# Performance work log

Measured on AMD Instinct MI355X. Metric: run time of the kernel, lower is better.

Reference implementation:

```python
import jax, jax.numpy as jnp
import numpy as np

BN_EPS = 1e-5


def setup_inputs() -> dict:
    key = jax.random.key(0)
    ks = jax.random.split(key, 6)
    b, c_out, c_high = 8, 256, 512
    h1 = w1 = 64
    h2 = w2 = 32
    return {
        "fms_low": jax.random.normal(ks[0], (b, c_out, h1, w1), jnp.float32),
        "fms_high": jax.random.normal(ks[1], (b, c_high, h2, w2), jnp.float32),
        "w_conv": jax.random.normal(ks[2], (c_out, c_high), jnp.float32) * (1.0 / np.sqrt(c_high)),
        "bn_gamma": jnp.ones((c_out,), jnp.float32),
        "bn_beta": jnp.zeros((c_out,), jnp.float32),
        "bn_mean": jnp.zeros((c_out,), jnp.float32),
        "bn_var": jnp.ones((c_out,), jnp.float32),
        "fc1_w": jax.random.normal(ks[3], (c_out // 4, c_out), jnp.float32) * (1.0 / np.sqrt(c_out)),
        "fc1_b": jnp.zeros((c_out // 4,), jnp.float32),
        "fc2_w": jax.random.normal(ks[4], (c_out // 4, c_out), jnp.float32) * (1.0 / np.sqrt(c_out)),
        "fc2_b": jnp.zeros((c_out // 4,), jnp.float32),
        "scale": jax.random.normal(ks[5], (1,), jnp.float32),
    }


def reference(fms_low, fms_high, w_conv, bn_gamma, bn_beta, bn_mean, bn_var,
              fc1_w, fc1_b, fc2_w, fc2_b, scale):
    b, c, h1, w1 = fms_low.shape
    # conv_high: 1x1 conv (no bias) + BN (inference) + ReLU
    x = jnp.einsum('bchw,oc->bohw', fms_high, w_conv)  # [b, 256, h2, w2]
    inv = bn_gamma / jnp.sqrt(bn_var + BN_EPS)
    x = x * inv[None, :, None, None] + (bn_beta - bn_mean * inv)[None, :, None, None]
    x = jax.nn.relu(x)
    # raw row-major reshapes, matching torch .view(b, -1, C)
    feat_low = fms_low.reshape(b, -1, c)    # [b, N_low, 256]
    feat_high = x.reshape(b, -1, c)         # [b, N_high, 256]
    mid_low = feat_low @ fc1_w.T + fc1_b    # [b, N_low, 64]
    mid_high = feat_high @ fc2_w.T + fc2_b  # [b, N_high, 64]
    energy = jnp.einsum('bnd,bmd->bnm', mid_low, mid_high)  # [b, N_low, N_high]
    attn = jax.nn.softmax(energy, axis=-1)
    # bmm(feat_high^T, attn^T) -> [b, 256, N_low]
    mid = jnp.einsum('bmc,bnm->bcn', feat_high, attn).reshape(b, c, h1, w1)
    return scale[0] * mid
```

## Files before the change

kernel.cpp:

```cpp
#include <hip/hip_runtime.h>
#include <hip/hip_bf16.h>

typedef __bf16 v8bf __attribute__((ext_vector_type(8)));
typedef float  v4f  __attribute__((ext_vector_type(4)));

typedef __attribute__((address_space(3))) void       lds_vd;
typedef __attribute__((address_space(1))) const void gbl_vd;

#define MFMA16(a, b, c) __builtin_amdgcn_mfma_f32_16x16x32_bf16(a, b, c, 0, 0, 0)

__device__ __forceinline__ void split_hl(float v, __bf16* h, __bf16* l) {
    __bf16 hh = (__bf16)v;
    *h = hh;
    *l = (__bf16)(v - (float)hh);
}

__device__ __forceinline__ int swz_idx(int row, int col) {
    return row * 64 + ((((col >> 3) ^ (row & 7))) << 3) + (col & 7);
}
__device__ __forceinline__ const __bf16* frag_ptr(const __bf16* base, int row, int g) {
    return base + row * 64 + ((g ^ (row & 7)) << 3);
}


__global__ __launch_bounds__(256) void k_conv(
    const float* __restrict__ FH, const float* __restrict__ W,
    const float* __restrict__ gamma, const float* __restrict__ beta,
    const float* __restrict__ mean, const float* __restrict__ var,
    __bf16* __restrict__ Xhi, __bf16* __restrict__ Xlo, __bf16* __restrict__ VT)
{
    __shared__ __align__(16) __bf16 Ah[2][64 * 64];
    __shared__ __align__(16) __bf16 Al[2][64 * 64];
    __shared__ __align__(16) __bf16 Bh[2][64 * 64];
    __shared__ __align__(16) __bf16 Bl[2][64 * 64];
    __shared__ float invl[64], shl[64];

    const int tid = threadIdx.x, lane = tid & 63, w = tid >> 6;
    const int l15 = lane & 15, quad = lane >> 4;
    const int u0 = blockIdx.x * 16, o0 = blockIdx.y * 64, b = blockIdx.z;
    const float* FHb = FH + (size_t)b * 524288;

    if (tid < 64) {
        const int o = o0 + tid;
        const float iv = gamma[o] * rsqrtf(var[o] + 1e-5f);
        invl[tid] = iv;
        shl[tid] = beta[o] - mean[o] * iv;
    }

    const int ao = tid >> 2, aseg = tid & 3;
    float wreg[16], freg[16];
    {
        const float* wp = W + (size_t)(o0 + ao) * 512 + aseg * 16;
        #pragma unroll
        for (int q = 0; q < 4; ++q) {
            float4 f = ((const float4*)wp)[q];
            wreg[4*q] = f.x; wreg[4*q+1] = f.y; wreg[4*q+2] = f.z; wreg[4*q+3] = f.w;
        }
        const float* fp = FHb + (size_t)lane * 1024 + w * 256 + u0;
        #pragma unroll
        for (int q = 0; q < 4; ++q) {
            float4 f = ((const float4*)fp)[q];
            freg[4*q] = f.x; freg[4*q+1] = f.y; freg[4*q+2] = f.z; freg[4*q+3] = f.w;
        }
    }

    v4f acc[2][2];
    #pragma unroll
    for (int i = 0; i < 2; ++i)
        #pragma unroll
        for (int j = 0; j < 2; ++j) { v4f z = {0.f,0.f,0.f,0.f}; acc[i][j] = z; }
    const int oh = w >> 1, nh = w & 1;

    for (int ch = 0; ch < 8; ++ch) {
        const int bf = ch & 1;
        #pragma unroll
        for (int z = 0; z < 2; ++z) {
            v8bf hv, lv;
            #pragma unroll
            for (int e = 0; e < 8; ++e) {
                __bf16 h, l; split_hl(wreg[8*z + e], &h, &l);
                hv[e] = h; lv[e] = l;
            }
            const int gi = (2*aseg + z) ^ (ao & 7);
            *(v8bf*)(Ah[bf] + ao*64 + (gi << 3)) = hv;
            *(v8bf*)(Al[bf] + ao*64 + (gi << 3)) = lv;
        }
        #pragma unroll
        for (int ul = 0; ul < 16; ++ul) {
            __bf16 h, l; split_hl(freg[ul], &h, &l);
            const int idx = (w*16 + ul)*64 + (((lane >> 3) ^ (ul & 7)) << 3) + (lane & 7);
            Bh[bf][idx] = h; Bl[bf][idx] = l;
        }
        __syncthreads();
        if (ch < 7) {
            const int c1 = (ch + 1) * 64;
            const float* wp = W + (size_t)(o0 + ao) * 512 + c1 + aseg * 16;
            #pragma unroll
            for (int q = 0; q < 4; ++q) {
                float4 f = ((const float4*)wp)[q];
                wreg[4*q] = f.x; wreg[4*q+1] = f.y; wreg[4*q+2] = f.z; wreg[4*q+3] = f.w;
            }
            const float* fp = FHb + (size_t)(c1 + lane) * 1024 + w * 256 + u0;
            #pragma unroll
            for (int q = 0; q < 4; ++q) {
                float4 f = ((const float4*)fp)[q];
                freg[4*q] = f.x; freg[4*q+1] = f.y; freg[4*q+2] = f.z; freg[4*q+3] = f.w;
            }
        }
        #pragma unroll
        for (int ks = 0; ks < 2; ++ks) {
            const int g = 4*ks + quad;
            v8bf a_h[2], a_l[2], b_h[2], b_l[2];
            #pragma unroll
            for (int i = 0; i < 2; ++i) {
                const int row = oh*32 + i*16 + l15;
                a_h[i] = *(const v8bf*)frag_ptr(Ah[bf], row, g);
                a_l[i] = *(const v8bf*)frag_ptr(Al[bf], row, g);
            }
            #pragma unroll
            for (int j = 0; j < 2; ++j) {
                const int row = nh*32 + j*16 + l15;
                b_h[j] = *(const v8bf*)frag_ptr(Bh[bf], row, g);
                b_l[j] = *(const v8bf*)frag_ptr(Bl[bf], row, g);
            }
            #pragma unroll
            for (int i = 0; i < 2; ++i)
                #pragma unroll
                for (int j = 0; j < 2; ++j) {
                    acc[i][j] = MFMA16(a_h[i], b_h[j], acc[i][j]);
                    acc[i][j] = MFMA16(a_h[i], b_l[j], acc[i][j]);
                    acc[i][j] = MFMA16(a_l[i], b_h[j], acc[i][j]);
                }
        }
    }
    __syncthreads();

    #pragma unroll
    for (int i = 0; i < 2; ++i)
        #pragma unroll
        for (int j = 0; j < 2; ++j)
            #pragma unroll
            for (int r = 0; r < 4; ++r) {
                const int row = oh*32 + i*16 + quad*4 + r;
                const int col = nh*32 + j*16 + l15;
                float v = acc[i][j][r] * invl[row] + shl[row];
                v = fmaxf(v, 0.f);
                __bf16 h, l; split_hl(v, &h, &l);
                const int idx = swz_idx(row, col);
                Ah[0][idx] = h; Al[0][idx] = l;
            }
    __syncthreads();
    {
        const int o = tid >> 2, pv = tid & 3;
        const size_t gbase = ((size_t)b*256 + o0 + o) * 1024 + pv*256 + u0;
        #pragma unroll
        for (int z = 0; z < 2; ++z) {
            const int gi = (2*pv + z) ^ (o & 7);
            v8bf h = *(v8bf*)(Ah[0] + o*64 + (gi << 3));
            v8bf l = *(v8bf*)(Al[0] + o*64 + (gi << 3));
            *(v8bf*)(Xhi + gbase + z*8) = h;
            *(v8bf*)(Xlo + gbase + z*8) = l;
        }
    }
    {
        const int ul = tid >> 4, s = tid & 15;
        __bf16 tmp[16];
        #pragma unroll
        for (int k = 0; k < 16; ++k) {
            const int m = s*16 + k;
            const int row = m >> 2;
            const int col = (m & 3)*16 + ul;
            tmp[k] = Ah[0][swz_idx(row, col)];
        }
        __bf16* vp = VT + ((size_t)b*256 + u0 + ul) * 1024 + 4*o0 + s*16;
        *(v8bf*)(vp)     = *(v8bf*)(tmp);
        *(v8bf*)(vp + 8) = *(v8bf*)(tmp + 8);
    }
}

__global__ __launch_bounds__(256) void k_proj32(
    const float* __restrict__ Feat, const float* __restrict__ Wfc,
    const float* __restrict__ bfc,
    __bf16* __restrict__ Ohi, __bf16* __restrict__ Olo)
{
    __shared__ __align__(16) __bf16 Wh[64 * 256], Wl[64 * 256];
    const int tid = threadIdx.x, lane = tid & 63, w = tid >> 6;
    const int l15 = lane & 15, quad = lane >> 4;
    const int r0 = blockIdx.x * 64;

    {
        const int row = tid >> 2, seg = tid & 3;
        const float* wp = Wfc + (size_t)row * 256 + seg * 64;
        #pragma unroll
        for (int z = 0; z < 8; ++z) {
            float4 f0 = ((const float4*)wp)[2*z];
            float4 f1 = ((const float4*)wp)[2*z + 1];
            float e[8] = {f0.x, f0.y, f0.z, f0.w, f1.x, f1.y, f1.z, f1.w};
            v8bf hv, lv;
            #pragma unroll
            for (int k = 0; k < 8; ++k) { __bf16 h, l; split_hl(e[k], &h, &l); hv[k] = h; lv[k] = l; }
            const int slot = (seg*8 + z) ^ (row & 7);
            *(v8bf*)(Wh + row*256 + (slot << 3)) = hv;
            *(v8bf*)(Wl + row*256 + (slot << 3)) = lv;
        }
    }
    __syncthreads();

    const float* ap = Feat + (size_t)(r0 + w*16 + l15) * 256;
    v4f acc[4];
    #pragma unroll
    for (int j = 0; j < 4; ++j) { v4f z = {0.f,0.f,0.f,0.f}; acc[j] = z; }

    #pragma unroll
    for (int ks = 0; ks < 8; ++ks) {
        float4 f0 = *(const float4*)(ap + ks*32 + quad*8);
        float4 f1 = *(const float4*)(ap + ks*32 + quad*8 + 4);
        float e[8] = {f0.x, f0.y, f0.z, f0.w, f1.x, f1.y, f1.z, f1.w};
        v8bf ah, al;
        #pragma unroll
        for (int k = 0; k < 8; ++k) { __bf16 h, l; split_hl(e[k], &h, &l); ah[k] = h; al[k] = l; }
        const int gk = ks*4 + quad;
        #pragma unroll
        for (int j = 0; j < 4; ++j) {
            const int row = j*16 + l15;
            const int slot = gk ^ (row & 7);
            v8bf bh = *(const v8bf*)(Wh + row*256 + (slot << 3));
            v8bf bl = *(const v8bf*)(Wl + row*256 + (slot << 3));
            acc[j] = MFMA16(ah, bh, acc[j]);
            acc[j] = MFMA16(ah, bl, acc[j]);
            acc[j] = MFMA16(al, bh, acc[j]);
        }
    }
    #pragma unroll
    for (int j = 0; j < 4; ++j) {
        const float bias = bfc[j*16 + l15];
        #pragma unroll
        for (int r = 0; r < 4; ++r) {
            const int orow = r0 + w*16 + quad*4 + r;
            __bf16 h, l; split_hl(acc[j][r] + bias, &h, &l);
            Ohi[(size_t)orow*64 + j*16 + l15] = h;
            Olo[(size_t)orow*64 + j*16 + l15] = l;
        }
    }
}

__global__ __launch_bounds__(256) void k_projbf(
    const __bf16* __restrict__ Fhi, const __bf16* __restrict__ Flo,
    const float* __restrict__ Wfc, const float* __restrict__ bfc,
    __bf16* __restrict__ Ohi, __bf16* __restrict__ Olo)
{
    __shared__ __align__(16) __bf16 Wh[64 * 256], Wl[64 * 256];
    const int tid = threadIdx.x, lane = tid & 63, w = tid >> 6;
    const int l15 = lane & 15, quad = lane >> 4;
    const int r0 = blockIdx.x * 64;

    {
        const int row = tid >> 2, seg = tid & 3;
        const float* wp = Wfc + (size_t)row * 256 + seg * 64;
        #pragma unroll
        for (int z = 0; z < 8; ++z) {
            float4 f0 = ((const float4*)wp)[2*z];
            float4 f1 = ((const float4*)wp)[2*z + 1];
            float e[8] = {f0.x, f0.y, f0.z, f0.w, f1.x, f1.y, f1.z, f1.w};
            v8bf hv, lv;
            #pragma unroll
            for (int k = 0; k < 8; ++k) { __bf16 h, l; split_hl(e[k], &h, &l); hv[k] = h; lv[k] = l; }
            const int slot = (seg*8 + z) ^ (row & 7);
            *(v8bf*)(Wh + row*256 + (slot << 3)) = hv;
            *(v8bf*)(Wl + row*256 + (slot << 3)) = lv;
        }
    }
    __syncthreads();

    const __bf16* aph = Fhi + (size_t)(r0 + w*16 + l15) * 256;
    const __bf16* apl = Flo + (size_t)(r0 + w*16 + l15) * 256;
    v4f acc[4];
    #pragma unroll
    for (int j = 0; j < 4; ++j) { v4f z = {0.f,0.f,0.f,0.f}; acc[j] = z; }

    #pragma unroll
    for (int ks = 0; ks < 8; ++ks) {
        v8bf ah = *(const v8bf*)(aph + ks*32 + quad*8);
        v8bf al = *(const v8bf*)(apl + ks*32 + quad*8);
        const int gk = ks*4 + quad;
        #pragma unroll
        for (int j = 0; j < 4; ++j) {
            const int row = j*16 + l15;
            const int slot = gk ^ (row & 7);
            v8bf bh = *(const v8bf*)(Wh + row*256 + (slot << 3));
            v8bf bl = *(const v8bf*)(Wl + row*256 + (slot << 3));
            acc[j] = MFMA16(ah, bh, acc[j]);
            acc[j] = MFMA16(ah, bl, acc[j]);
            acc[j] = MFMA16(al, bh, acc[j]);
        }
    }
    #pragma unroll
    for (int j = 0; j < 4; ++j) {
        const float bias = bfc[j*16 + l15];
        #pragma unroll
        for (int r = 0; r < 4; ++r) {
            const int orow = r0 + w*16 + quad*4 + r;
            __bf16 h, l; split_hl(acc[j][r] + bias, &h, &l);
            Ohi[(size_t)orow*64 + j*16 + l15] = h;
            Olo[(size_t)orow*64 + j*16 + l15] = l;
        }
    }
}

__global__ __launch_bounds__(256) void k_attn(
    const __bf16* __restrict__ MLhi, const __bf16* __restrict__ MLlo,
    const __bf16* __restrict__ MHhi, const __bf16* __restrict__ MHlo,
    const __bf16* __restrict__ VT,
    const float* __restrict__ scale_p,
    float* __restrict__ out)
{
    __shared__ __align__(16) __bf16 Khi[2][32 * 64];
    __shared__ __align__(16) __bf16 Klo[2][32 * 64];
    __shared__ __align__(16) __bf16 Vs[2][256 * 32];

    const int tid = threadIdx.x, lane = tid & 63, w = tid >> 6;
    const int l15 = lane & 15, quad = lane >> 4;
    const int b = blockIdx.x & 7, qtb = blockIdx.x >> 3;
    const int q0 = qtb * 64;

    v8bf qhi[2], qlo[2];
    {
        const __bf16* qp  = MLhi + ((size_t)(b*4096 + q0 + w*16 + l15)) * 64;
        const __bf16* qlp = MLlo + ((size_t)(b*4096 + q0 + w*16 + l15)) * 64;
        #pragma unroll
        for (int h = 0; h < 2; ++h) {
            qhi[h] = *(const v8bf*)(qp + h*32 + quad*8);
            qlo[h] = *(const v8bf*)(qlp + h*32 + quad*8);
        }
    }

    const char* Khg = (const char*)(MHhi + (size_t)b * 65536);
    const char* Klg = (const char*)(MHlo + (size_t)b * 65536);
    const char* Vg  = (const char*)(VT + (size_t)b * 262144);
    const int offK = (lane >> 3) * 128 + (((lane & 7) ^ ((lane >> 3) & 7)) << 4);
    const int offV = (lane >> 2) * 2048 + ((((lane & 3) ^ ((lane >> 3) & 3))) << 4);

    v4f oacc[16];
    #pragma unroll
    for (int ct = 0; ct < 16; ++ct) { v4f z = {0.f,0.f,0.f,0.f}; oacc[ct] = z; }
    float lrow = 0.f;

    const int srcA = l15 + (((2*quad) & 3) << 4);
    const int srcB = l15 + (((2*quad + 1) & 3) << 4);
    const bool hi_mb = ((quad >> 1) & 1) != 0;

    {
        __builtin_amdgcn_global_load_lds((gbl_vd*)(Khg + w*1024 + offK),
                                         (lds_vd*)((char*)Khi[0] + w*1024), 16, 0, 0);
        __builtin_amdgcn_global_load_lds((gbl_vd*)(Klg + w*1024 + offK),
                                         (lds_vd*)((char*)Klo[0] + w*1024), 16, 0, 0);
        for (int i = w; i < 16; i += 4)
            __builtin_amdgcn_global_load_lds((gbl_vd*)(Vg + i*32768 + offV),
                                             (lds_vd*)((char*)Vs[0] + i*1024), 16, 0, 0);
    }

    for (int ch = 0; ch < 32; ++ch) {
        const int bf = ch & 1;
        __syncthreads();
        if (ch < 31) {
            const int m0 = (ch + 1) * 32, nb = bf ^ 1;
            __builtin_amdgcn_global_load_lds((gbl_vd*)(Khg + m0*128 + w*1024 + offK),
                                             (lds_vd*)((char*)Khi[nb] + w*1024), 16, 0, 0);
            __builtin_amdgcn_global_load_lds((gbl_vd*)(Klg + m0*128 + w*1024 + offK),
                                             (lds_vd*)((char*)Klo[nb] + w*1024), 16, 0, 0);
            for (int i = w; i < 16; i += 4)
                __builtin_amdgcn_global_load_lds((gbl_vd*)(Vg + m0*2 + i*32768 + offV),
                                                 (lds_vd*)((char*)Vs[nb] + i*1024), 16, 0, 0);
        }

        v4f s0 = {0.f,0.f,0.f,0.f}, s1 = {0.f,0.f,0.f,0.f};
        #pragma unroll
        for (int h = 0; h < 2; ++h) {
            const int g = h*4 + quad;
            v8bf kh0 = *(const v8bf*)frag_ptr(Khi[bf], l15,      g);
            v8bf kl0 = *(const v8bf*)frag_ptr(Klo[bf], l15,      g);
            v8bf kh1 = *(const v8bf*)frag_ptr(Khi[bf], 16 + l15, g);
            v8bf kl1 = *(const v8bf*)frag_ptr(Klo[bf], 16 + l15, g);
            s0 = MFMA16(kh0, qhi[h], s0);
            s0 = MFMA16(kl0, qhi[h], s0);
            s0 = MFMA16(kh0, qlo[h], s0);
            s1 = MFMA16(kh1, qhi[h], s1);
            s1 = MFMA16(kl1, qhi[h], s1);
            s1 = MFMA16(kh1, qlo[h], s1);
        }

        float P0[4], P1[4];
        #pragma unroll
        for (int r = 0; r < 4; ++r) {
            P0[r] = __expf(s0[r]);
            P1[r] = __expf(s1[r]);
            lrow += P0[r] + P1[r];
        }

        v8bf pf;
        #pragma unroll
        for (int r = 0; r < 4; ++r) {
            const float a0 = __shfl(P0[r], srcA, 64);
            const float a1 = __shfl(P1[r], srcA, 64);
            pf[r] = (__bf16)(hi_mb ? a1 : a0);
            const float b0 = __shfl(P0[r], srcB, 64);
            const float b1 = __shfl(P1[r], srcB, 64);
            pf[4 + r] = (__bf16)(hi_mb ? b1 : b0);
        }

        #pragma unroll
        for (int ct = 0; ct < 16; ++ct) {
            const int vrow = ct*16 + l15;
            v8bf vv = *(const v8bf*)(Vs[bf] + vrow*32 + ((quad ^ ((vrow >> 1) & 3)) << 3));
            oacc[ct] = MFMA16(vv, pf, oacc[ct]);
        }
    }

    lrow += __shfl_xor(lrow, 16, 64);
    lrow += __shfl_xor(lrow, 32, 64);
    const float invq = scale_p[0] / lrow;

    float* outb = out + (size_t)b * 256 * 4096 + q0 + w*16 + l15;
    #pragma unroll
    for (int ct = 0; ct < 16; ++ct) {
        #pragma unroll
        for (int r = 0; r < 4; ++r) {
            const int c = ct*16 + quad*4 + r;
            outb[(size_t)c * 4096] = oacc[ct][r] * invq;
        }
    }
}

extern "C" void kernel_launch(void* const* d_in, const int* in_sizes, int n_in,
                              void* d_out, int out_size, void* d_ws, size_t ws_size,
                              hipStream_t stream)
{
    const float* fms_low  = (const float*)d_in[0];
    const float* fms_high = (const float*)d_in[1];
    const float* w_conv   = (const float*)d_in[2];
    const float* gamma    = (const float*)d_in[3];
    const float* beta     = (const float*)d_in[4];
    const float* mean     = (const float*)d_in[5];
    const float* var      = (const float*)d_in[6];
    const float* fc1_w    = (const float*)d_in[7];
    const float* fc1_b    = (const float*)d_in[8];
    const float* fc2_w    = (const float*)d_in[9];
    const float* fc2_b    = (const float*)d_in[10];
    const float* scale    = (const float*)d_in[11];
    float* out = (float*)d_out;

    __bf16* Xhi  = (__bf16*)d_ws;
    __bf16* Xlo  = Xhi  + (size_t)8*256*1024;
    __bf16* VT   = Xlo  + (size_t)8*256*1024;
    __bf16* MLhi = VT   + (size_t)8*256*1024;
    __bf16* MLlo = MLhi + (size_t)8*4096*64;
    __bf16* MHhi = MLlo + (size_t)8*4096*64;
    __bf16* MHlo = MHhi + (size_t)8*1024*64;

    k_conv<<<dim3(16, 4, 8), 256, 0, stream>>>(fms_high, w_conv, gamma, beta,
                                               mean, var, Xhi, Xlo, VT);
    k_projbf<<<dim3(128), 256, 0, stream>>>(Xhi, Xlo, fc2_w, fc2_b, MHhi, MHlo);
    k_proj32<<<dim3(512), 256, 0, stream>>>(fms_low, fc1_w, fc1_b, MLhi, MLlo);
    k_attn<<<dim3(512), 256, 0, stream>>>(MLhi, MLlo, MHhi, MHlo, VT, scale, out);
}
```

Baseline: 197.0 us.

## Merge conv and low projection into one launch, split attention over channel halves

The conv+BN+ReLU kernel and the fc1 projection of the low-resolution features are merged into one kernel, with the block index choosing the role. The conv loses its LDS double buffer, and the fc1 weights are staged in two K chunks to shrink LDS. The high projection now uses 32-row blocks, doubling its grid. Attention splits the 256 output channels into two halves per block, doubling the grid and halving accumulators and V staging. This trades more occupancy and parallelism for recomputing QK^T and the softmax in both channel halves, and drops one kernel launch.

```diff
diff --git a/kernel.cpp b/kernel.cpp
--- a/kernel.cpp
+++ b/kernel.cpp
@@ -23,223 +23,227 @@
 }
 
 
-__global__ __launch_bounds__(256) void k_conv(
+__global__ __launch_bounds__(256) void k_prep(
     const float* __restrict__ FH, const float* __restrict__ W,
     const float* __restrict__ gamma, const float* __restrict__ beta,
     const float* __restrict__ mean, const float* __restrict__ var,
-    __bf16* __restrict__ Xhi, __bf16* __restrict__ Xlo, __bf16* __restrict__ VT)
+    const float* __restrict__ Feat,
+    const float* __restrict__ fc1w, const float* __restrict__ fc1b,
+    __bf16* __restrict__ Xhi, __bf16* __restrict__ Xlo, __bf16* __restrict__ VT,
+    __bf16* __restrict__ MLhi, __bf16* __restrict__ MLlo)
 {
-    __shared__ __align__(16) __bf16 Ah[2][64 * 64];
-    __shared__ __align__(16) __bf16 Al[2][64 * 64];
-    __shared__ __align__(16) __bf16 Bh[2][64 * 64];
-    __shared__ __align__(16) __bf16 Bl[2][64 * 64];
-    __shared__ float invl[64], shl[64];
-
+    __shared__ __align__(16) char smem[33280];
     const int tid = threadIdx.x, lane = tid & 63, w = tid >> 6;
     const int l15 = lane & 15, quad = lane >> 4;
-    const int u0 = blockIdx.x * 16, o0 = blockIdx.y * 64, b = blockIdx.z;
-    const float* FHb = FH + (size_t)b * 524288;
-
-    if (tid < 64) {
-        const int o = o0 + tid;
-        const float iv = gamma[o] * rsqrtf(var[o] + 1e-5f);
-        invl[tid] = iv;
-        shl[tid] = beta[o] - mean[o] * iv;
-    }
-
-    const int ao = tid >> 2, aseg = tid & 3;
-    float wreg[16], freg[16];
-    {
-        const float* wp = W + (size_t)(o0 + ao) * 512 + aseg * 16;
-        #pragma unroll
-        for (int q = 0; q < 4; ++q) {
-            float4 f = ((const float4*)wp)[q];
-            wreg[4*q] = f.x; wreg[4*q+1] = f.y; wreg[4*q+2] = f.z; wreg[4*q+3] = f.w;
-        }
-        const float* fp = FHb + (size_t)lane * 1024 + w * 256 + u0;
-        #pragma unroll
-        for (int q = 0; q < 4; ++q) {
-            float4 f = ((const float4*)fp)[q];
-            freg[4*q] = f.x; freg[4*q+1] = f.y; freg[4*q+2] = f.z; freg[4*q+3] = f.w;
-        }
-    }
-
-    v4f acc[2][2];
-    #pragma unroll
-    for (int i = 0; i < 2; ++i)
-        #pragma unroll
-        for (int j = 0; j < 2; ++j) { v4f z = {0.f,0.f,0.f,0.f}; acc[i][j] = z; }
-    const int oh = w >> 1, nh = w & 1;
-
-    for (int ch = 0; ch < 8; ++ch) {
-        const int bf = ch & 1;
-        #pragma unroll
-        for (int z = 0; z < 2; ++z) {
-            v8bf hv, lv;
-            #pragma unroll
-            for (int e = 0; e < 8; ++e) {
-                __bf16 h, l; split_hl(wreg[8*z + e], &h, &l);
-                hv[e] = h; lv[e] = l;
-            }
-            const int gi = (2*aseg + z) ^ (ao & 7);
-            *(v8bf*)(Ah[bf] + ao*64 + (gi << 3)) = hv;
-            *(v8bf*)(Al[bf] + ao*64 + (gi << 3)) = lv;
-        }
-        #pragma unroll
-        for (int ul = 0; ul < 16; ++ul) {
-            __bf16 h, l; split_hl(freg[ul], &h, &l);
-            const int idx = (w*16 + ul)*64 + (((lane >> 3) ^ (ul & 7)) << 3) + (lane & 7);
-            Bh[bf][idx] = h; Bl[bf][idx] = l;
-        }
-        __syncthreads();
-        if (ch < 7) {
-            const int c1 = (ch + 1) * 64;
-            const float* wp = W + (size_t)(o0 + ao) * 512 + c1 + aseg * 16;
+    const int bid = blockIdx.x;
+
+    if (bid < 512) {
+        __bf16* Ah = (__bf16*)smem;
+        __bf16* Al = (__bf16*)(smem + 8192);
+        __bf16* Bh = (__bf16*)(smem + 16384);
+        __bf16* Bl = (__bf16*)(smem + 24576);
+        float* invl = (float*)(smem + 32768);
+        float* shl  = (float*)(smem + 33024);
+
+        const int u0 = (bid & 15) * 16, o0 = ((bid >> 4) & 3) * 64, b = bid >> 6;
+        const float* FHb = FH + (size_t)b * 524288;
+
+        if (tid < 64) {
+            const int o = o0 + tid;
+            const float iv = gamma[o] * rsqrtf(var[o] + 1e-5f);
+            invl[tid] = iv;
+            shl[tid] = beta[o] - mean[o] * iv;
+        }
+
+        const int ao = tid >> 2, aseg = tid & 3;
+        float wreg[16], freg[16];
+        {
+            const float* wp = W + (size_t)(o0 + ao) * 512 + aseg * 16;
             #pragma unroll
             for (int q = 0; q < 4; ++q) {
                 float4 f = ((const float4*)wp)[q];
                 wreg[4*q] = f.x; wreg[4*q+1] = f.y; wreg[4*q+2] = f.z; wreg[4*q+3] = f.w;
             }
-            const float* fp = FHb + (size_t)(c1 + lane) * 1024 + w * 256 + u0;
+            const float* fp = FHb + (size_t)lane * 1024 + w * 256 + u0;
             #pragma unroll
             for (int q = 0; q < 4; ++q) {
                 float4 f = ((const float4*)fp)[q];
                 freg[4*q] = f.x; freg[4*q+1] = f.y; freg[4*q+2] = f.z; freg[4*q+3] = f.w;
             }
         }
-        #pragma unroll
-        for (int ks = 0; ks < 2; ++ks) {
-            const int g = 4*ks + quad;
-            v8bf a_h[2], a_l[2], b_h[2], b_l[2];
-            #pragma unroll
-            for (int i = 0; i < 2; ++i) {
-                const int row = oh*32 + i*16 + l15;
-                a_h[i] = *(const v8bf*)frag_ptr(Ah[bf], row, g);
-                a_l[i] = *(const v8bf*)frag_ptr(Al[bf], row, g);
-            }
-            #pragma unroll
-            for (int j = 0; j < 2; ++j) {
-                const int row = nh*32 + j*16 + l15;
-                b_h[j] = *(const v8bf*)frag_ptr(Bh[bf], row, g);
-                b_l[j] = *(const v8bf*)frag_ptr(Bl[bf], row, g);
-            }
-            #pragma unroll
-            for (int i = 0; i < 2; ++i)
+
+        v4f acc[2][2];
+        #pragma unroll
+        for (int i = 0; i < 2; ++i)
+            #pragma unroll
+            for (int j = 0; j < 2; ++j) { v4f z = {0.f,0.f,0.f,0.f}; acc[i][j] = z; }
+        const int oh = w >> 1, nh = w & 1;
+
+        for (int ch = 0; ch < 8; ++ch) {
+            if (ch) __syncthreads();
+            #pragma unroll
+            for (int z = 0; z < 2; ++z) {
+                v8bf hv, lv;
+                #pragma unroll
+                for (int e = 0; e < 8; ++e) {
+                    __bf16 h, l; split_hl(wreg[8*z + e], &h, &l);
+                    hv[e] = h; lv[e] = l;
+                }
+                const int gi = (2*aseg + z) ^ (ao & 7);
+                *(v8bf*)(Ah + ao*64 + (gi << 3)) = hv;
+                *(v8bf*)(Al + ao*64 + (gi << 3)) = lv;
+            }
+            #pragma unroll
+            for (int ul = 0; ul < 16; ++ul) {
+                __bf16 h, l; split_hl(freg[ul], &h, &l);
+                const int idx = (w*16 + ul)*64 + (((lane >> 3) ^ (ul & 7)) << 3) + (lane & 7);
+                Bh[idx] = h; Bl[idx] = l;
+            }
+            __syncthreads();
+            if (ch < 7) {
+                const int c1 = (ch + 1) * 64;
+                const float* wp = W + (size_t)(o0 + ao) * 512 + c1 + aseg * 16;
+                #pragma unroll
+                for (int q = 0; q < 4; ++q) {
+                    float4 f = ((const float4*)wp)[q];
+                    wreg[4*q] = f.x; wreg[4*q+1] = f.y; wreg[4*q+2] = f.z; wreg[4*q+3] = f.w;
+                }
+                const float* fp = FHb + (size_t)(c1 + lane) * 1024 + w * 256 + u0;
+                #pragma unroll
+                for (int q = 0; q < 4; ++q) {
+                    float4 f = ((const float4*)fp)[q];
+                    freg[4*q] = f.x; freg[4*q+1] = f.y; freg[4*q+2] = f.z; freg[4*q+3] = f.w;
+                }
+            }
+            #pragma unroll
+            for (int ks = 0; ks < 2; ++ks) {
+                const int g = 4*ks + quad;
+                v8bf a_h[2], a_l[2], b_h[2], b_l[2];
+                #pragma unroll
+                for (int i = 0; i < 2; ++i) {
+                    const int row = oh*32 + i*16 + l15;
+                    a_h[i] = *(const v8bf*)frag_ptr(Ah, row, g);
+                    a_l[i] = *(const v8bf*)frag_ptr(Al, row, g);
+                }
                 #pragma unroll
                 for (int j = 0; j < 2; ++j) {
-                    acc[i][j] = MFMA16(a_h[i], b_h[j], acc[i][j]);
-                    acc[i][j] = MFMA16(a_h[i], b_l[j], acc[i][j]);
-                    acc[i][j] = MFMA16(a_l[i], b_h[j], acc[i][j]);
-                }
-        }
-    }
-    __syncthreads();
-
-    #pragma unroll
-    for (int i = 0; i < 2; ++i)
-        #pragma unroll
-        for (int j = 0; j < 2; ++j)
+                    const int row = nh*32 + j*16 + l15;
+                    b_h[j] = *(const v8bf*)frag_ptr(Bh, row, g);
+                    b_l[j] = *(const v8bf*)frag_ptr(Bl, row, g);
+                }
+                #pragma unroll
+                for (int i = 0; i < 2; ++i)
+                    #pragma unroll
+                    for (int j = 0; j < 2; ++j) {
+                        acc[i][j] = MFMA16(a_h[i], b_h[j], acc[i][j]);
+                        acc[i][j] = MFMA16(a_h[i], b_l[j], acc[i][j]);
+                        acc[i][j] = MFMA16(a_l[i], b_h[j], acc[i][j]);
+                    }
+            }
+        }
+        __syncthreads();
+
+        #pragma unroll
+        for (int i = 0; i < 2; ++i)
+            #pragma unroll
+            for (int j = 0; j < 2; ++j)
+                #pragma unroll
+                for (int r = 0; r < 4; ++r) {
+                    const int row = oh*32 + i*16 + quad*4 + r;
+                    const int col = nh*32 + j*16 + l15;
+                    float v = acc[i][j][r] * invl[row] + shl[row];
+                    v = fmaxf(v, 0.f);
+                    __bf16 h, l; split_hl(v, &h, &l);
+                    const int idx = swz_idx(row, col);
+                    Ah[idx] = h; Al[idx] = l;
+                }
+        __syncthreads();
+        {
+            const int o = tid >> 2, pv = tid & 3;
+            const size_t gbase = ((size_t)b*256 + o0 + o) * 1024 + pv*256 + u0;
+            #pragma unroll
+            for (int z = 0; z < 2; ++z) {
+                const int gi = (2*pv + z) ^ (o & 7);
+                v8bf h = *(v8bf*)(Ah + o*64 + (gi << 3));
+                v8bf l = *(v8bf*)(Al + o*64 + (gi << 3));
+                *(v8bf*)(Xhi + gbase + z*8) = h;
+                *(v8bf*)(Xlo + gbase + z*8) = l;
+            }
+        }
+        {
+            const int ul = tid >> 4, s = tid & 15;
+            __bf16 tmp[16];
+            #pragma unroll
+            for (int k = 0; k < 16; ++k) {
+                const int m = s*16 + k;
+                const int row = m >> 2;
+                const int col = (m & 3)*16 + ul;
+                tmp[k] = Ah[swz_idx(row, col)];
+            }
+            __bf16* vp = VT + ((size_t)b*256 + u0 + ul) * 1024 + 4*(bid >> 4 & 3)*64 + s*16;
+            *(v8bf*)(vp)     = *(v8bf*)(tmp);
+            *(v8bf*)(vp + 8) = *(v8bf*)(tmp + 8);
+        }
+    } else {
+        __bf16* Wh = (__bf16*)smem;
+        __bf16* Wl = (__bf16*)(smem + 16384);
+        const int r0 = (bid - 512) * 64;
+        const float* ap = Feat + (size_t)(r0 + w*16 + l15) * 256;
+
+        v4f acc[4];
+        #pragma unroll
+        for (int j = 0; j < 4; ++j) { v4f z = {0.f,0.f,0.f,0.f}; acc[j] = z; }
+
+        for (int kc = 0; kc < 2; ++kc) {
+            if (kc) __syncthreads();
+            {
+                const int row = tid >> 2, seg = tid & 3;
+                const float* wp = fc1w + (size_t)row * 256 + kc*128 + seg * 32;
+                #pragma unroll
+                for (int z = 0; z < 4; ++z) {
+                    float4 f0 = ((const float4*)wp)[2*z];
+                    float4 f1 = ((const float4*)wp)[2*z + 1];
+                    float e[8] = {f0.x, f0.y, f0.z, f0.w, f1.x, f1.y, f1.z, f1.w};
+                    v8bf hv, lv;
+                    #pragma unroll
+                    for (int k = 0; k < 8; ++k) { __bf16 h, l; split_hl(e[k], &h, &l); hv[k] = h; lv[k] = l; }
+                    const int slot = (seg*4 + z) ^ (row & 7);
+                    *(v8bf*)(Wh + row*128 + (slot << 3)) = hv;
+                    *(v8bf*)(Wl + row*128 + (slot << 3)) = lv;
+                }
+            }
+            __syncthreads();
+            #pragma unroll
+            for (int ks = 0; ks < 4; ++ks) {
+                float4 f0 = *(const float4*)(ap + kc*128 + ks*32 + quad*8);
+                float4 f1 = *(const float4*)(ap + kc*128 + ks*32 + quad*8 + 4);
+                float e[8] = {f0.x, f0.y, f0.z, f0.w, f1.x, f1.y, f1.z, f1.w};
+                v8bf ah, al;
+                #pragma unroll
+                for (int k = 0; k < 8; ++k) { __bf16 h, l; split_hl(e[k], &h, &l); ah[k] = h; al[k] = l; }
+                const int gk = ks*4 + quad;
+                #pragma unroll
+                for (int j = 0; j < 4; ++j) {
+                    const int row = j*16 + l15;
+                    const int slot = gk ^ (row & 7);
+                    v8bf bh = *(const v8bf*)(Wh + row*128 + (slot << 3));
+                    v8bf bl = *(const v8bf*)(Wl + row*128 + (slot << 3));
+                    acc[j] = MFMA16(ah, bh, acc[j]);
+                    acc[j] = MFMA16(ah, bl, acc[j]);
+                    acc[j] = MFMA16(al, bh, acc[j]);
+                }
+            }
+        }
+        #pragma unroll
+        for (int j = 0; j < 4; ++j) {
+            const float bias = fc1b[j*16 + l15];
             #pragma unroll
             for (int r = 0; r < 4; ++r) {
-                const int row = oh*32 + i*16 + quad*4 + r;
-                const int col = nh*32 + j*16 + l15;
-                float v = acc[i][j][r] * invl[row] + shl[row];
-                v = fmaxf(v, 0.f);
-                __bf16 h, l; split_hl(v, &h, &l);
-                const int idx = swz_idx(row, col);
-                Ah[0][idx] = h; Al[0][idx] = l;
-            }
-    __syncthreads();
-    {
-        const int o = tid >> 2, pv = tid & 3;
-        const size_t gbase = ((size_t)b*256 + o0 + o) * 1024 + pv*256 + u0;
-        #pragma unroll
-        for (int z = 0; z < 2; ++z) {
-            const int gi = (2*pv + z) ^ (o & 7);
-            v8bf h = *(v8bf*)(Ah[0] + o*64 + (gi << 3));
-            v8bf l = *(v8bf*)(Al[0] + o*64 + (gi << 3));
-            *(v8bf*)(Xhi + gbase + z*8) = h;
-            *(v8bf*)(Xlo + gbase + z*8) = l;
-        }
-    }
-    {
-        const int ul = tid >> 4, s = tid & 15;
-        __bf16 tmp[16];
-        #pragma unroll
-        for (int k = 0; k < 16; ++k) {
-            const int m = s*16 + k;
-            const int row = m >> 2;
-            const int col = (m & 3)*16 + ul;
-            tmp[k] = Ah[0][swz_idx(row, col)];
-        }
-        __bf16* vp = VT + ((size_t)b*256 + u0 + ul) * 1024 + 4*o0 + s*16;
-        *(v8bf*)(vp)     = *(v8bf*)(tmp);
-        *(v8bf*)(vp + 8) = *(v8bf*)(tmp + 8);
-    }
-}
-
-__global__ __launch_bounds__(256) void k_proj32(
-    const float* __restrict__ Feat, const float* __restrict__ Wfc,
-    const float* __restrict__ bfc,
-    __bf16* __restrict__ Ohi, __bf16* __restrict__ Olo)
-{
-    __shared__ __align__(16) __bf16 Wh[64 * 256], Wl[64 * 256];
-    const int tid = threadIdx.x, lane = tid & 63, w = tid >> 6;
-    const int l15 = lane & 15, quad = lane >> 4;
-    const int r0 = blockIdx.x * 64;
-
-    {
-        const int row = tid >> 2, seg = tid & 3;
-        const float* wp = Wfc + (size_t)row * 256 + seg * 64;
-        #pragma unroll
-        for (int z = 0; z < 8; ++z) {
-            float4 f0 = ((const float4*)wp)[2*z];
-            float4 f1 = ((const float4*)wp)[2*z + 1];
-            float e[8] = {f0.x, f0.y, f0.z, f0.w, f1.x, f1.y, f1.z, f1.w};
-            v8bf hv, lv;
-            #pragma unroll
-            for (int k = 0; k < 8; ++k) { __bf16 h, l; split_hl(e[k], &h, &l); hv[k] = h; lv[k] = l; }
-            const int slot = (seg*8 + z) ^ (row & 7);
-            *(v8bf*)(Wh + row*256 + (slot << 3)) = hv;
-            *(v8bf*)(Wl + row*256 + (slot << 3)) = lv;
-        }
-    }
-    __syncthreads();
-
-    const float* ap = Feat + (size_t)(r0 + w*16 + l15) * 256;
-    v4f acc[4];
-    #pragma unroll
-    for (int j = 0; j < 4; ++j) { v4f z = {0.f,0.f,0.f,0.f}; acc[j] = z; }
-
-    #pragma unroll
-    for (int ks = 0; ks < 8; ++ks) {
-        float4 f0 = *(const float4*)(ap + ks*32 + quad*8);
-        float4 f1 = *(const float4*)(ap + ks*32 + quad*8 + 4);
-        float e[8] = {f0.x, f0.y, f0.z, f0.w, f1.x, f1.y, f1.z, f1.w};
-        v8bf ah, al;
-        #pragma unroll
-        for (int k = 0; k < 8; ++k) { __bf16 h, l; split_hl(e[k], &h, &l); ah[k] = h; al[k] = l; }
-        const int gk = ks*4 + quad;
-        #pragma unroll
-        for (int j = 0; j < 4; ++j) {
-            const int row = j*16 + l15;
-            const int slot = gk ^ (row & 7);
-            v8bf bh = *(const v8bf*)(Wh + row*256 + (slot << 3));
-            v8bf bl = *(const v8bf*)(Wl + row*256 + (slot << 3));
-            acc[j] = MFMA16(ah, bh, acc[j]);
-            acc[j] = MFMA16(ah, bl, acc[j]);
-            acc[j] = MFMA16(al, bh, acc[j]);
-        }
-    }
-    #pragma unroll
-    for (int j = 0; j < 4; ++j) {
-        const float bias = bfc[j*16 + l15];
-        #pragma unroll
-        for (int r = 0; r < 4; ++r) {
-            const int orow = r0 + w*16 + quad*4 + r;
-            __bf16 h, l; split_hl(acc[j][r] + bias, &h, &l);
-            Ohi[(size_t)orow*64 + j*16 + l15] = h;
-            Olo[(size_t)orow*64 + j*16 + l15] = l;
+                const int orow = r0 + w*16 + quad*4 + r;
+                __bf16 h, l; split_hl(acc[j][r] + bias, &h, &l);
+                MLhi[(size_t)orow*64 + j*16 + l15] = h;
+                MLlo[(size_t)orow*64 + j*16 + l15] = l;
+            }
         }
     }
 }
@@ -249,60 +253,63 @@
     const float* __restrict__ Wfc, const float* __restrict__ bfc,
     __bf16* __restrict__ Ohi, __bf16* __restrict__ Olo)
 {
-    __shared__ __align__(16) __bf16 Wh[64 * 256], Wl[64 * 256];
+    __shared__ __align__(16) __bf16 Wh[64 * 128], Wl[64 * 128];
     const int tid = threadIdx.x, lane = tid & 63, w = tid >> 6;
     const int l15 = lane & 15, quad = lane >> 4;
-    const int r0 = blockIdx.x * 64;
-
-    {
-        const int row = tid >> 2, seg = tid & 3;
-        const float* wp = Wfc + (size_t)row * 256 + seg * 64;
-        #pragma unroll
-        for (int z = 0; z < 8; ++z) {
-            float4 f0 = ((const float4*)wp)[2*z];
-            float4 f1 = ((const float4*)wp)[2*z + 1];
-            float e[8] = {f0.x, f0.y, f0.z, f0.w, f1.x, f1.y, f1.z, f1.w};
-            v8bf hv, lv;
-            #pragma unroll
-            for (int k = 0; k < 8; ++k) { __bf16 h, l; split_hl(e[k], &h, &l); hv[k] = h; lv[k] = l; }
-            const int slot = (seg*8 + z) ^ (row & 7);
-            *(v8bf*)(Wh + row*256 + (slot << 3)) = hv;
-            *(v8bf*)(Wl + row*256 + (slot << 3)) = lv;
-        }
-    }
-    __syncthreads();
-
-    const __bf16* aph = Fhi + (size_t)(r0 + w*16 + l15) * 256;
-    const __bf16* apl = Flo + (size_t)(r0 + w*16 + l15) * 256;
-    v4f acc[4];
+    const int r0 = blockIdx.x * 32;
+    const int mt = w & 1, dh = w >> 1;
+
+    const __bf16* aph = Fhi + (size_t)(r0 + mt*16 + l15) * 256;
+    const __bf16* apl = Flo + (size_t)(r0 + mt*16 + l15) * 256;
+
+    v4f acc[2];
+    { v4f z = {0.f,0.f,0.f,0.f}; acc[0] = z; acc[1] = z; }
+
+    for (int kc = 0; kc < 2; ++kc) {
+        if (kc) __syncthreads();
+        {
+            const int row = tid >> 2, seg = tid & 3;
+            const float* wp = Wfc + (size_t)row * 256 + kc*128 + seg * 32;
+            #pragma unroll
+            for (int z = 0; z < 4; ++z) {
+                float4 f0 = ((const float4*)wp)[2*z];
+                float4 f1 = ((const float4*)wp)[2*z + 1];
+                float e[8] = {f0.x, f0.y, f0.z, f0.w, f1.x, f1.y, f1.z, f1.w};
+                v8bf hv, lv;
+                #pragma unroll
+                for (int k = 0; k < 8; ++k) { __bf16 h, l; split_hl(e[k], &h, &l); hv[k] = h; lv[k] = l; }
+                const int slot = (seg*4 + z) ^ (row & 7);
+                *(v8bf*)(Wh + row*128 + (slot << 3)) = hv;
+                *(v8bf*)(Wl + row*128 + (slot << 3)) = lv;
+            }
+        }
+        __syncthreads();
+        #pragma unroll
+        for (int ks = 0; ks < 4; ++ks) {
+            v8bf ah = *(const v8bf*)(aph + kc*128 + ks*32 + quad*8);
+            v8bf al = *(const v8bf*)(apl + kc*128 + ks*32 + quad*8);
+            const int gk = ks*4 + quad;
+            #pragma unroll
+            for (int j = 0; j < 2; ++j) {
+                const int row = (dh*2 + j)*16 + l15;
+                const int slot = gk ^ (row & 7);
+                v8bf bh = *(const v8bf*)(Wh + row*128 + (slot << 3));
+                v8bf bl = *(const v8bf*)(Wl + row*128 + (slot << 3));
+                acc[j] = MFMA16(ah, bh, acc[j]);
+                acc[j] = MFMA16(ah, bl, acc[j]);
+                acc[j] = MFMA16(al, bh, acc[j]);
+            }
+        }
+    }
     #pragma unroll
-    for (int j = 0; j < 4; ++j) { v4f z = {0.f,0.f,0.f,0.f}; acc[j] = z; }
-
-    #pragma unroll
-    for (int ks = 0; ks < 8; ++ks) {
-        v8bf ah = *(const v8bf*)(aph + ks*32 + quad*8);
-        v8bf al = *(const v8bf*)(apl + ks*32 + quad*8);
-        const int gk = ks*4 + quad;
-        #pragma unroll
-        for (int j = 0; j < 4; ++j) {
-            const int row = j*16 + l15;
-            const int slot = gk ^ (row & 7);
-            v8bf bh = *(const v8bf*)(Wh + row*256 + (slot << 3));
-            v8bf bl = *(const v8bf*)(Wl + row*256 + (slot << 3));
-            acc[j] = MFMA16(ah, bh, acc[j]);
-            acc[j] = MFMA16(ah, bl, acc[j]);
-            acc[j] = MFMA16(al, bh, acc[j]);
-        }
-    }
-    #pragma unroll
-    for (int j = 0; j < 4; ++j) {
-        const float bias = bfc[j*16 + l15];
+    for (int j = 0; j < 2; ++j) {
+        const float bias = bfc[(dh*2 + j)*16 + l15];
         #pragma unroll
         for (int r = 0; r < 4; ++r) {
-            const int orow = r0 + w*16 + quad*4 + r;
+            const int orow = r0 + mt*16 + quad*4 + r;
             __bf16 h, l; split_hl(acc[j][r] + bias, &h, &l);
-            Ohi[(size_t)orow*64 + j*16 + l15] = h;
-            Olo[(size_t)orow*64 + j*16 + l15] = l;
+            Ohi[(size_t)orow*64 + (dh*2 + j)*16 + l15] = h;
+            Olo[(size_t)orow*64 + (dh*2 + j)*16 + l15] = l;
         }
     }
 }
@@ -316,12 +323,14 @@
 {
     __shared__ __align__(16) __bf16 Khi[2][32 * 64];
     __shared__ __align__(16) __bf16 Klo[2][32 * 64];
-    __shared__ __align__(16) __bf16 Vs[2][256 * 32];
+    __shared__ __align__(16) __bf16 Vs[2][128 * 32];
 
     const int tid = threadIdx.x, lane = tid & 63, w = tid >> 6;
     const int l15 = lane & 15, quad = lane >> 4;
-    const int b = blockIdx.x & 7, qtb = blockIdx.x >> 3;
-    const int q0 = qtb * 64;
+    const int b = blockIdx.x & 7;
+    const int t = blockIdx.x >> 3;
+    const int q0 = (t >> 1) * 64;
+    const int c0 = (t & 1) * 128;
 
     v8bf qhi[2], qlo[2];
     {
@@ -336,13 +345,13 @@
 
     const char* Khg = (const char*)(MHhi + (size_t)b * 65536);
     const char* Klg = (const char*)(MHlo + (size_t)b * 65536);
-    const char* Vg  = (const char*)(VT + (size_t)b * 262144);
+    const char* Vg  = (const char*)(VT + (size_t)b * 262144) + (size_t)c0 * 2048;
     const int offK = (lane >> 3) * 128 + (((lane & 7) ^ ((lane >> 3) & 7)) << 4);
     const int offV = (lane >> 2) * 2048 + ((((lane & 3) ^ ((lane >> 3) & 3))) << 4);
 
-    v4f oacc[16];
+    v4f oacc[8];
     #pragma unroll
-    for (int ct = 0; ct < 16; ++ct) { v4f z = {0.f,0.f,0.f,0.f}; oacc[ct] = z; }
+    for (int ct = 0; ct < 8; ++ct) { v4f z = {0.f,0.f,0.f,0.f}; oacc[ct] = z; }
     float lrow = 0.f;
 
     const int srcA = l15 + (((2*quad) & 3) << 4);
@@ -354,7 +363,8 @@
                                          (lds_vd*)((char*)Khi[0] + w*1024), 16, 0, 0);
         __builtin_amdgcn_global_load_lds((gbl_vd*)(Klg + w*1024 + offK),
                                          (lds_vd*)((char*)Klo[0] + w*1024), 16, 0, 0);
-        for (int i = w; i < 16; i += 4)
+        #pragma unroll
+        for (int i = w; i < 8; i += 4)
             __builtin_amdgcn_global_load_lds((gbl_vd*)(Vg + i*32768 + offV),
                                              (lds_vd*)((char*)Vs[0] + i*1024), 16, 0, 0);
     }
@@ -368,7 +378,8 @@
                                              (lds_vd*)((char*)Khi[nb] + w*1024), 16, 0, 0);
             __builtin_amdgcn_global_load_lds((gbl_vd*)(Klg + m0*128 + w*1024 + offK),
                                              (lds_vd*)((char*)Klo[nb] + w*1024), 16, 0, 0);
-            for (int i = w; i < 16; i += 4)
+            #pragma unroll
+            for (int i = w; i < 8; i += 4)
                 __builtin_amdgcn_global_load_lds((gbl_vd*)(Vg + m0*2 + i*32768 + offV),
                                                  (lds_vd*)((char*)Vs[nb] + i*1024), 16, 0, 0);
         }
@@ -409,7 +420,7 @@
         }
 
         #pragma unroll
-        for (int ct = 0; ct < 16; ++ct) {
+        for (int ct = 0; ct < 8; ++ct) {
             const int vrow = ct*16 + l15;
             v8bf vv = *(const v8bf*)(Vs[bf] + vrow*32 + ((quad ^ ((vrow >> 1) & 3)) << 3));
             oacc[ct] = MFMA16(vv, pf, oacc[ct]);
@@ -422,10 +433,10 @@
 
     float* outb = out + (size_t)b * 256 * 4096 + q0 + w*16 + l15;
     #pragma unroll
-    for (int ct = 0; ct < 16; ++ct) {
+    for (int ct = 0; ct < 8; ++ct) {
         #pragma unroll
         for (int r = 0; r < 4; ++r) {
-            const int c = ct*16 + quad*4 + r;
+            const int c = c0 + ct*16 + quad*4 + r;
             outb[(size_t)c * 4096] = oacc[ct][r] * invq;
         }
     }
@@ -457,9 +468,9 @@
     __bf16* MHhi = MLlo + (size_t)8*4096*64;
     __bf16* MHlo = MHhi + (size_t)8*1024*64;
 
-    k_conv<<<dim3(16, 4, 8), 256, 0, stream>>>(fms_high, w_conv, gamma, beta,
-                                               mean, var, Xhi, Xlo, VT);
-    k_projbf<<<dim3(128), 256, 0, stream>>>(Xhi, Xlo, fc2_w, fc2_b, MHhi, MHlo);
-    k_proj32<<<dim3(512), 256, 0, stream>>>(fms_low, fc1_w, fc1_b, MLhi, MLlo);
-    k_attn<<<dim3(512), 256, 0, stream>>>(MLhi, MLlo, MHhi, MHlo, VT, scale, out);
-}
+    k_prep<<<dim3(1024), 256, 0, stream>>>(fms_high, w_conv, gamma, beta, mean, var,
+                                           fms_low, fc1_w, fc1_b,
+                                           Xhi, Xlo, VT, MLhi, MLlo);
+    k_projbf<<<dim3(256), 256, 0, stream>>>(Xhi, Xlo, fc2_w, fc2_b, MHhi, MHlo);
+    k_attn<<<dim3(1024), 256, 0, stream>>>(MLhi, MLlo, MHhi, MHlo, VT, scale, out);
+}
```

New measurement: 207.3 us. +5.2%, slower.
